# Optimization experiments

Hardware: AMD Instinct MI355X
Metric: run time of the kernel (lower is better)

## Reference

```python
import jax, jax.numpy as jnp
import numpy as np

B, N, E0, F_IN, H, EMB, VEC, DPI = 1024, 256, 2048, 6, 32, 32, 26, 512


def setup_inputs() -> dict:
    key = jax.random.key(0)
    ks = jax.random.split(key, 16)
    # fixed urban scene graph, shared by every batch element, with self-loops
    src0 = jax.random.randint(ks[0], (E0,), 0, N, dtype=jnp.int32)
    dst0 = jax.random.randint(ks[1], (E0,), 0, N, dtype=jnp.int32)
    loops = jnp.arange(N, dtype=jnp.int32)
    src = jnp.concatenate([src0, loops])
    dst = jnp.concatenate([dst0, loops])

    s = 0.05
    return {
        "graph_feats": jax.random.normal(ks[2], (B, N, F_IN), jnp.float32),
        "vector": jax.random.normal(ks[3], (B, VEC), jnp.float32),
        "src": src,
        "dst": dst,
        "W1": jax.random.normal(ks[4], (F_IN, H), jnp.float32) * s,
        "b1": jnp.zeros((H,), jnp.float32),
        "W2": jax.random.normal(ks[5], (H, H), jnp.float32) * s,
        "b2": jnp.zeros((H,), jnp.float32),
        "W3": jax.random.normal(ks[6], (H, H), jnp.float32) * s,
        "b3": jnp.zeros((H,), jnp.float32),
        "W_emb": jax.random.normal(ks[7], (H, EMB), jnp.float32) * s,
        "b_emb": jnp.zeros((EMB,), jnp.float32),
        "W_pi": jax.random.normal(ks[8], (VEC + EMB, DPI), jnp.float32) * s,
        "b_pi": jnp.zeros((DPI,), jnp.float32),
        "W_vf": jax.random.normal(ks[9], (VEC + EMB, DPI), jnp.float32) * s,
        "b_vf": jnp.zeros((DPI,), jnp.float32),
    }


def _edge_norm(src, dst, n_nodes):
    # DGL GraphConv norm='both': out_deg(src)^-1/2 * in_deg(dst)^-1/2
    ones = jnp.ones(src.shape[0], jnp.float32)
    deg_out = jax.ops.segment_sum(ones, src, num_segments=n_nodes)
    deg_in = jax.ops.segment_sum(ones, dst, num_segments=n_nodes)
    inv_o = jnp.where(deg_out > 0, deg_out ** -0.5, 0.0)
    inv_i = jnp.where(deg_in > 0, deg_in ** -0.5, 0.0)
    return inv_o[src] * inv_i[dst]  # [E]


def _gconv(h, src, dst, norm, W, b):
    # h: [B, N, F]; symmetric-normalized aggregation then linear (DGL GraphConv)
    msg = h[:, src, :] * norm[None, :, None]          # [B, E, F]
    agg = jnp.zeros_like(h).at[:, dst, :].add(msg)     # [B, N, F]
    return agg @ W + b


def reference(graph_feats, vector, src, dst, W1, b1, W2, b2, W3, b3,
              W_emb, b_emb, W_pi, b_pi, W_vf, b_vf):
    n_nodes = graph_feats.shape[1]
    norm = _edge_norm(src, dst, n_nodes)
    h = jax.nn.relu(_gconv(graph_feats, src, dst, norm, W1, b1))
    h = jax.nn.relu(_gconv(h, src, dst, norm, W2, b2))
    h = jax.nn.relu(_gconv(h, src, dst, norm, W3, b3))  # three_layers=True
    hg = jnp.mean(h, axis=1)                 # dgl.mean_nodes -> [B, H]
    emb = hg @ W_emb + b_emb                 # [B, EMB]
    comb = jnp.concatenate([vector[:, :26], emb], axis=1)  # [B, 58]
    pi = jax.nn.relu(comb @ W_pi + b_pi)
    vf = jax.nn.relu(comb @ W_vf + b_vf)
    return pi, vf
```

## Files before the change

### kernel.cpp

```cpp
#include <hip/hip_runtime.h>
#include <hip/hip_fp16.h>

#define B_    1024
#define N_    256
#define E_    2304
#define EPT_  9
#define FIN_  6
#define VEC_  26
#define HSTR_ 40

__global__ __launch_bounds__(256) void fused_kernel(
    const float* __restrict__ gf,
    const float* __restrict__ vec,
    const int* __restrict__ src, const int* __restrict__ dst,
    const float* __restrict__ W1, const float* __restrict__ b1,
    const float* __restrict__ W2, const float* __restrict__ b2,
    const float* __restrict__ W3, const float* __restrict__ b3,
    const float* __restrict__ We, const float* __restrict__ be,
    const float* __restrict__ Wpi, const float* __restrict__ bpi,
    const float* __restrict__ Wvf, const float* __restrict__ bvf,
    float2* __restrict__ out)
{
    __shared__ __align__(16) __half hbuf[N_ * HSTR_];
    __shared__ unsigned int packedE[E_];
    __shared__ float part[8 * 33];
    __shared__ float hgl[32];
    __shared__ float comb[VEC_ + 32];
    __shared__ int   wsum[4];

    const int t = threadIdx.x;
    const int b = blockIdx.x;
    const int lane = t & 63, wv = t >> 6;

    int*   deg_o  = (int*)hbuf;
    int*   deg_i  = (int*)hbuf + 256;
    int*   scanA  = (int*)hbuf + 512;
    int*   cursor = (int*)hbuf + 768;
    int*   perm   = (int*)hbuf + 1024;
    float* inv_o  = (float*)hbuf + 1280;
    float* inv_i  = (float*)hbuf + 1536;
    int*   bcnt   = (int*)hbuf + 1792;
    int*   boff   = (int*)hbuf + 1856;

    deg_o[t] = 0; deg_i[t] = 0;
    if (t < 64) bcnt[t] = 0;
    __syncthreads();

    int sB[EPT_], dB[EPT_];
#pragma unroll
    for (int i = 0; i < EPT_; ++i) { int e = t + 256 * i; sB[i] = src[e]; dB[i] = dst[e]; }
#pragma unroll
    for (int i = 0; i < EPT_; ++i) { atomicAdd(&deg_o[sB[i]], 1); atomicAdd(&deg_i[dB[i]], 1); }
    __syncthreads();

    const int dI = deg_i[t];
    {
        int dO = deg_o[t];
        inv_o[t] = dO > 0 ? rsqrtf((float)dO) : 0.f;
        inv_i[t] = dI > 0 ? rsqrtf((float)dI) : 0.f;
    }
    int x = dI;
#pragma unroll
    for (int d = 1; d < 64; d <<= 1) {
        int y = __shfl_up(x, d, 64);
        if (lane >= d) x += y;
    }
    if (lane == 63) wsum[wv] = x;
    const int bucket = dI > 63 ? 63 : dI;
    atomicAdd(&bcnt[bucket], 1);
    __syncthreads();

    {
        int prefix = 0;
#pragma unroll
        for (int w = 0; w < 3; ++w) if (w < wv) prefix += wsum[w];
        int incl = x + prefix;
        scanA[t]  = incl;
        cursor[t] = incl - dI;
    }
    if (t < 64) {
        int c = bcnt[t], xx = c;
#pragma unroll
        for (int d = 1; d < 64; d <<= 1) {
            int y = __shfl_up(xx, d, 64);
            if (lane >= d) xx += y;
        }
        boff[t] = xx - c;
    }
    __syncthreads();

    { int pos = atomicAdd(&boff[bucket], 1); perm[pos] = t; }
#pragma unroll
    for (int i = 0; i < EPT_; ++i) {
        int s = sB[i], dd = dB[i];
        int pos = atomicAdd(&cursor[dd], 1);
        float nrm = inv_o[s] * inv_i[dd];
        unsigned short h = __half_as_ushort(__float2half(nrm));
        packedE[pos] = ((unsigned int)s << 16) | (unsigned int)h;
    }
    __syncthreads();

    const int node = perm[t];
    const int end  = scanA[node];
    const int beg  = end - deg_i[node];
    __syncthreads();

    {
        const float* g = gf + (size_t)b * (N_ * FIN_);
        for (int i = t; i < N_ * 8; i += 256) {
            int n = i >> 3, k = i & 7;
            hbuf[n * HSTR_ + k] = __float2half((k < FIN_) ? g[n * FIN_ + k] : 0.f);
        }
    }
    __syncthreads();

    const __half2 z2 = __float2half2_rn(0.f);
    float o[32];

    {
        __half2 a2[4] = {z2, z2, z2, z2};
        for (int e = beg; e < end; ++e) {
            unsigned int u = packedE[e];
            __half2 w2 = __half2half2(__ushort_as_half((unsigned short)(u & 0xffffu)));
            union { float4 f4; __half2 h2[4]; } r;
            r.f4 = *(const float4*)&hbuf[(u >> 16) * HSTR_];
#pragma unroll
            for (int q = 0; q < 4; ++q) a2[q] = __hfma2(w2, r.h2[q], a2[q]);
        }
        float a[FIN_];
#pragma unroll
        for (int k = 0; k < FIN_; ++k)
            a[k] = (k & 1) ? __high2float(a2[k >> 1]) : __low2float(a2[k >> 1]);
#pragma unroll
        for (int j = 0; j < 32; ++j) o[j] = b1[j];
#pragma unroll
        for (int k = 0; k < FIN_; ++k) {
            float ak = a[k];
            const float* wr = &W1[k * 32];
#pragma unroll
            for (int j = 0; j < 32; ++j) o[j] += ak * wr[j];
        }
#pragma unroll
        for (int j = 0; j < 32; ++j) o[j] = fmaxf(o[j], 0.f);
    }
    __syncthreads();
    {
        union { float4 f4; __half2 h2[4]; } w;
        float4* row = (float4*)&hbuf[node * HSTR_];
#pragma unroll
        for (int q = 0; q < 4; ++q) {
#pragma unroll
            for (int r = 0; r < 4; ++r)
                w.h2[r] = __floats2half2_rn(o[8 * q + 2 * r], o[8 * q + 2 * r + 1]);
            row[q] = w.f4;
        }
    }
    __syncthreads();

    for (int L = 0; L < 2; ++L) {
        __half2 acc2[16];
#pragma unroll
        for (int j = 0; j < 16; ++j) acc2[j] = z2;
        for (int e = beg; e < end; ++e) {
            unsigned int u = packedE[e];
            __half2 w2 = __half2half2(__ushort_as_half((unsigned short)(u & 0xffffu)));
            const float4* hr = (const float4*)&hbuf[(u >> 16) * HSTR_];
            union { float4 f4; __half2 h2[4]; } r0, r1, r2, r3;
            r0.f4 = hr[0]; r1.f4 = hr[1]; r2.f4 = hr[2]; r3.f4 = hr[3];
#pragma unroll
            for (int q = 0; q < 4; ++q) {
                acc2[q]      = __hfma2(w2, r0.h2[q], acc2[q]);
                acc2[4 + q]  = __hfma2(w2, r1.h2[q], acc2[4 + q]);
                acc2[8 + q]  = __hfma2(w2, r2.h2[q], acc2[8 + q]);
                acc2[12 + q] = __hfma2(w2, r3.h2[q], acc2[12 + q]);
            }
        }
        float a[32];
#pragma unroll
        for (int i = 0; i < 16; ++i) {
            a[2 * i]     = __low2float(acc2[i]);
            a[2 * i + 1] = __high2float(acc2[i]);
        }
        const float* Wl = (L == 0) ? W2 : W3;
        const float* Bl = (L == 0) ? b2 : b3;
#pragma unroll
        for (int j = 0; j < 32; ++j) o[j] = Bl[j];
#pragma unroll 8
        for (int k = 0; k < 32; ++k) {
            float ak = a[k];
            const float* wr = &Wl[k * 32];
#pragma unroll
            for (int j = 0; j < 32; ++j) o[j] += ak * wr[j];
        }
#pragma unroll
        for (int j = 0; j < 32; ++j) o[j] = fmaxf(o[j], 0.f);
        __syncthreads();
        {
            union { float4 f4; __half2 h2[4]; } w;
            float4* row = (float4*)&hbuf[node * HSTR_];
#pragma unroll
            for (int q = 0; q < 4; ++q) {
#pragma unroll
                for (int r = 0; r < 4; ++r)
                    w.h2[r] = __floats2half2_rn(o[8 * q + 2 * r], o[8 * q + 2 * r + 1]);
                row[q] = w.f4;
            }
        }
        __syncthreads();
    }

    {
        int j = t & 31, g8 = t >> 5;
        float s = 0.f;
        for (int i = 0; i < 32; ++i)
            s += __half2float(hbuf[(g8 * 32 + i) * HSTR_ + j]);
        part[g8 * 33 + j] = s;
    }
    __syncthreads();
    if (t < 32) {
        float sum = 0.f;
#pragma unroll
        for (int g8 = 0; g8 < 8; ++g8) sum += part[g8 * 33 + t];
        hgl[t] = sum * (1.0f / 256.0f);
    }
    __syncthreads();

    if (t < 32) {
        float v = be[t];
#pragma unroll
        for (int j = 0; j < 32; ++j) v += hgl[j] * We[j * 32 + t];
        comb[VEC_ + t] = v;
    }
    if (t < VEC_) comb[t] = vec[b * VEC_ + t];
    __syncthreads();

    {
        float p0 = bpi[2 * t], p1 = bpi[2 * t + 1];
        float v0 = bvf[2 * t], v1 = bvf[2 * t + 1];
        const float2* Wp = (const float2*)Wpi;
        const float2* Wv = (const float2*)Wvf;
        for (int k = 0; k < VEC_ + 32; ++k) {
            float c = comb[k];
            float2 a = Wp[k * 256 + t];
            p0 += c * a.x; p1 += c * a.y;
            float2 d = Wv[k * 256 + t];
            v0 += c * d.x; v1 += c * d.y;
        }
        out[b * 256 + t]          = make_float2(fmaxf(p0, 0.f), fmaxf(p1, 0.f));
        out[262144 + b * 256 + t] = make_float2(fmaxf(v0, 0.f), fmaxf(v1, 0.f));
    }
}

extern "C" void kernel_launch(void* const* d_in, const int* in_sizes, int n_in,
                              void* d_out, int out_size, void* d_ws, size_t ws_size,
                              hipStream_t stream)
{
    fused_kernel<<<B_, 256, 0, stream>>>(
        (const float*)d_in[0], (const float*)d_in[1],
        (const int*)d_in[2], (const int*)d_in[3],
        (const float*)d_in[4], (const float*)d_in[5],
        (const float*)d_in[6], (const float*)d_in[7],
        (const float*)d_in[8], (const float*)d_in[9],
        (const float*)d_in[10], (const float*)d_in[11],
        (const float*)d_in[12], (const float*)d_in[13],
        (const float*)d_in[14], (const float*)d_in[15],
        (float2*)d_out);
}
```

Measured before the change: 125.2 us.

## Use MFMA f16 matrix instructions for the 32x32 dense layers in GCN layers 2-3

The per-node 32x32 dense transform after aggregation is moved off scalar FMA loops. The aggregated half-precision features are first written back to shared memory, then each wave runs 16x16x32 f16 MFMA on a 64-node slab, with bias folded into the accumulator and ReLU applied on store. This removes about 1024 scalar FMAs per thread per layer and the large o/a register arrays, which should also lower register pressure. The cost is an extra shared-memory round trip and barrier per layer, and the weights are rounded to fp16 before the multiply.

```diff
diff --git a/kernel.cpp b/kernel.cpp
--- a/kernel.cpp
+++ b/kernel.cpp
@@ -8,6 +8,9 @@
 #define FIN_  6
 #define VEC_  26
 #define HSTR_ 40
+
+typedef _Float16 half8 __attribute__((ext_vector_type(8)));
+typedef float    f32x4 __attribute__((ext_vector_type(4)));
 
 __global__ __launch_bounds__(256) void fused_kernel(
     const float* __restrict__ gf,
@@ -115,7 +118,6 @@
     __syncthreads();
 
     const __half2 z2 = __float2half2_rn(0.f);
-    float o[32];
 
     {
         __half2 a2[4] = {z2, z2, z2, z2};
@@ -127,7 +129,7 @@
 #pragma unroll
             for (int q = 0; q < 4; ++q) a2[q] = __hfma2(w2, r.h2[q], a2[q]);
         }
-        float a[FIN_];
+        float a[FIN_], o[32];
 #pragma unroll
         for (int k = 0; k < FIN_; ++k)
             a[k] = (k & 1) ? __high2float(a2[k >> 1]) : __low2float(a2[k >> 1]);
@@ -140,24 +142,38 @@
 #pragma unroll
             for (int j = 0; j < 32; ++j) o[j] += ak * wr[j];
         }
-#pragma unroll
-        for (int j = 0; j < 32; ++j) o[j] = fmaxf(o[j], 0.f);
-    }
-    __syncthreads();
-    {
+        __syncthreads();
         union { float4 f4; __half2 h2[4]; } w;
         float4* row = (float4*)&hbuf[node * HSTR_];
 #pragma unroll
         for (int q = 0; q < 4; ++q) {
 #pragma unroll
             for (int r = 0; r < 4; ++r)
-                w.h2[r] = __floats2half2_rn(o[8 * q + 2 * r], o[8 * q + 2 * r + 1]);
+                w.h2[r] = __floats2half2_rn(fmaxf(o[8*q + 2*r], 0.f), fmaxf(o[8*q + 2*r + 1], 0.f));
             row[q] = w.f4;
         }
     }
     __syncthreads();
 
+    const int m16  = lane & 15;
+    const int q4   = lane >> 4;
+    const int slab = wv * 64;
+
     for (int L = 0; L < 2; ++L) {
+        const float* Wl = (L == 0) ? W2 : W3;
+        const float* Bl = (L == 0) ? b2 : b3;
+
+        half8 bfrag[2];
+        float bias_c[2];
+#pragma unroll
+        for (int h = 0; h < 2; ++h) {
+            int col = m16 + 16 * h;
+#pragma unroll
+            for (int j = 0; j < 8; ++j)
+                bfrag[h][j] = (_Float16)Wl[(q4 * 8 + j) * 32 + col];
+            bias_c[h] = Bl[col];
+        }
+
         __half2 acc2[16];
 #pragma unroll
         for (int j = 0; j < 16; ++j) acc2[j] = z2;
@@ -175,25 +191,6 @@
                 acc2[12 + q] = __hfma2(w2, r3.h2[q], acc2[12 + q]);
             }
         }
-        float a[32];
-#pragma unroll
-        for (int i = 0; i < 16; ++i) {
-            a[2 * i]     = __low2float(acc2[i]);
-            a[2 * i + 1] = __high2float(acc2[i]);
-        }
-        const float* Wl = (L == 0) ? W2 : W3;
-        const float* Bl = (L == 0) ? b2 : b3;
-#pragma unroll
-        for (int j = 0; j < 32; ++j) o[j] = Bl[j];
-#pragma unroll 8
-        for (int k = 0; k < 32; ++k) {
-            float ak = a[k];
-            const float* wr = &Wl[k * 32];
-#pragma unroll
-            for (int j = 0; j < 32; ++j) o[j] += ak * wr[j];
-        }
-#pragma unroll
-        for (int j = 0; j < 32; ++j) o[j] = fmaxf(o[j], 0.f);
         __syncthreads();
         {
             union { float4 f4; __half2 h2[4]; } w;
@@ -201,9 +198,37 @@
 #pragma unroll
             for (int q = 0; q < 4; ++q) {
 #pragma unroll
-                for (int r = 0; r < 4; ++r)
-                    w.h2[r] = __floats2half2_rn(o[8 * q + 2 * r], o[8 * q + 2 * r + 1]);
+                for (int r = 0; r < 4; ++r) w.h2[r] = acc2[4 * q + r];
                 row[q] = w.f4;
+            }
+        }
+        __syncthreads();
+
+        half8 afrag[4];
+#pragma unroll
+        for (int g = 0; g < 4; ++g) {
+            union { float4 f4; half8 h8; } u;
+            u.f4 = *(const float4*)&hbuf[(slab + g * 16 + m16) * HSTR_ + q4 * 8];
+            afrag[g] = u.h8;
+        }
+        f32x4 D[4][2];
+#pragma unroll
+        for (int g = 0; g < 4; ++g) {
+#pragma unroll
+            for (int h = 0; h < 2; ++h) {
+                f32x4 c = {bias_c[h], bias_c[h], bias_c[h], bias_c[h]};
+                D[g][h] = __builtin_amdgcn_mfma_f32_16x16x32_f16(afrag[g], bfrag[h], c, 0, 0, 0);
+            }
+        }
+#pragma unroll
+        for (int g = 0; g < 4; ++g) {
+#pragma unroll
+            for (int h = 0; h < 2; ++h) {
+#pragma unroll
+                for (int r = 0; r < 4; ++r) {
+                    float v = fmaxf(D[g][h][r], 0.f);
+                    hbuf[(slab + g * 16 + q4 * 4 + r) * HSTR_ + h * 16 + m16] = __float2half(v);
+                }
             }
         }
         __syncthreads();
```

Measured after the change: 117.2 us. 6.4% less time.
